# Kernel optimization log

Measured on AMD Instinct MI355X. Metric: run time of the kernel, lower is better.

Reference implementation:

```python
import jax, jax.numpy as jnp
import numpy as np

B, I, P, H = 256, 1024, 128, 128
L_PROT = 1024
ATOMS_PER_MOL = 128
N_LIG = B * ATOMS_PER_MOL  # 32768 total ligand atoms


def setup_inputs() -> dict:
    key = jax.random.key(0)
    ks = jax.random.split(key, 6)
    param_enc = jax.random.normal(ks[0], (B, I, P), dtype=jnp.float32)
    h_prot = jax.random.normal(ks[1], (B, L_PROT, H), dtype=jnp.float32)
    w1 = jax.random.normal(ks[2], (P, 1), dtype=jnp.float32) / np.sqrt(P)
    b1 = jax.random.normal(ks[3], (1,), dtype=jnp.float32)
    indices_lig = jax.random.randint(ks[4], (B, I), 0, ATOMS_PER_MOL)
    indices_prot = jax.random.randint(ks[5], (B, I), 0, L_PROT)
    protein_idx = jnp.arange(B)            # complex b -> protein row b
    lig_offsets = jnp.arange(B) * ATOMS_PER_MOL  # 'split' cumulative atom offsets
    mask = jnp.ones((B, I), dtype=bool)    # valid (non -510 padded) interactions
    return {
        "param_enc": param_enc, "h_prot": h_prot, "w1": w1, "b1": b1,
        "indices_lig": indices_lig, "indices_prot": indices_prot,
        "protein_idx": protein_idx, "lig_offsets": lig_offsets, "mask": mask,
    }


def reference(param_enc, h_prot, w1, b1, indices_lig, indices_prot,
              protein_idx, lig_offsets, mask):
    # scalar gate per interaction: ReLU(Linear(param_enc))  (dropout = identity, eval mode)
    gate = jax.nn.relu(jnp.einsum("bip,po->bio", param_enc, w1) + b1)  # [B, I, 1]
    # gather protein residue features: h_prot[protein_idx[b], indices_prot[b,i], :]
    gathered = h_prot[protein_idx[:, None], indices_prot]              # [B, I, H]
    contrib = gate * gathered * mask[..., None]                        # [B, I, H]
    # scatter-add into per-ligand-atom accumulator at split + i_l
    glob = (lig_offsets[:, None] + indices_lig).reshape(-1)            # [B*I]
    protein_inter = jnp.zeros((N_LIG, H), dtype=contrib.dtype)
    protein_inter = protein_inter.at[glob].add(contrib.reshape(-1, H))
    return protein_inter
```

## Files before the change

### kernel.cpp

```cpp
#include <hip/hip_runtime.h>

#define B_ 256
#define I_ 1024
#define P_ 128
#define H_ 128
#define LP_ 1024

__global__ __launch_bounds__(1024) void fused_ile(
    const float* __restrict__ param_enc,
    const float* __restrict__ h_prot,
    const float* __restrict__ w1,
    const float* __restrict__ b1,
    const int* __restrict__ indices_lig,
    const int* __restrict__ indices_prot,
    const int* __restrict__ protein_idx,
    const int* __restrict__ lig_offsets,
    float* __restrict__ out)
{
    __shared__ float          s_gate[I_];
    __shared__ unsigned short s_ip[I_];
    __shared__ unsigned short s_items[I_];
    __shared__ int            s_cnt[128];
    __shared__ int            s_start[129];
    __shared__ int            s_cur[128];

    const int tid  = threadIdx.x;
    const int b    = blockIdx.x;
    const int lane = tid & 63;
    const int wave = tid >> 6;
    const int half = lane >> 5;
    const int sub  = lane & 31;
    const int halfIdx = wave * 2 + half;

    if (tid < 128) s_cnt[tid] = 0;

    const float bias = b1[0];
    const int pb = protein_idx[b];
    const float4 wv = *(const float4*)(w1 + sub * 4);

    const float* pe_b = param_enc + (size_t)b * I_ * P_;
    const float* hp_b = h_prot + (size_t)pb * LP_ * H_;
    const int* il_b = indices_lig + b * I_;
    const int* ip_b = indices_prot + b * I_;

    #pragma unroll 8
    for (int q = 0; q < 32; ++q) {
        const int p  = wave + q * 16;
        const int i0 = p * 2;
        float4 pv = *(const float4*)(pe_b + (size_t)i0 * P_ + lane * 4);
        float part = pv.x * wv.x + pv.y * wv.y + pv.z * wv.z + pv.w * wv.w;
        part += __shfl_xor(part, 1);
        part += __shfl_xor(part, 2);
        part += __shfl_xor(part, 4);
        part += __shfl_xor(part, 8);
        part += __shfl_xor(part, 16);
        if (sub == 0) s_gate[i0 + half] = part + bias;
    }
    __syncthreads();

    const int  my_il = il_b[tid];
    const int  my_ip = ip_b[tid];
    const bool live  = s_gate[tid] > 0.f;
    s_ip[tid] = (unsigned short)my_ip;
    if (live) atomicAdd(&s_cnt[my_il], 1);
    __syncthreads();

    if (wave == 0) {
        const int c0 = s_cnt[2 * lane];
        const int c1 = s_cnt[2 * lane + 1];
        int s = c0 + c1;
        #pragma unroll
        for (int d = 1; d < 64; d <<= 1) {
            int t = __shfl_up(s, d);
            if (lane >= d) s += t;
        }
        s_start[2 * lane]     = s - c0 - c1;
        s_start[2 * lane + 1] = s - c1;
        if (lane == 63) s_start[128] = s;
    }
    __syncthreads();
    if (tid < 128) s_cur[tid] = s_start[tid];
    __syncthreads();

    if (live) {
        const int pos = atomicAdd(&s_cur[my_il], 1);
        s_items[pos] = (unsigned short)tid;
    }
    __syncthreads();

    const int base = lig_offsets[b];
    int st[4], cn[4];
    #pragma unroll
    for (int rr = 0; rr < 4; ++rr) {
        const int a = halfIdx + rr * 32;
        st[rr] = s_start[a];
        cn[rr] = s_start[a + 1] - st[rr];
    }
    float4 acc[4];
    #pragma unroll
    for (int rr = 0; rr < 4; ++rr) acc[rr] = make_float4(0.f, 0.f, 0.f, 0.f);

    int mx = max(max(cn[0], cn[1]), max(cn[2], cn[3]));
    for (int j = 0; j < mx; ++j) {
        #pragma unroll
        for (int rr = 0; rr < 4; ++rr) {
            if (j < cn[rr]) {
                const int   item = s_items[st[rr] + j];
                const float g    = s_gate[item];
                const int   ip   = s_ip[item];
                const float4 hv  = *(const float4*)(hp_b + (size_t)ip * H_ + sub * 4);
                acc[rr].x += g * hv.x;
                acc[rr].y += g * hv.y;
                acc[rr].z += g * hv.z;
                acc[rr].w += g * hv.w;
            }
        }
    }

    #pragma unroll
    for (int rr = 0; rr < 4; ++rr) {
        float* o = out + (size_t)(base + halfIdx + rr * 32) * H_;
        *(float4*)(o + sub * 4) = acc[rr];
    }
}

extern "C" void kernel_launch(void* const* d_in, const int* in_sizes, int n_in,
                              void* d_out, int out_size, void* d_ws, size_t ws_size,
                              hipStream_t stream) {
    const float* param_enc   = (const float*)d_in[0];
    const float* h_prot      = (const float*)d_in[1];
    const float* w1          = (const float*)d_in[2];
    const float* b1          = (const float*)d_in[3];
    const int* indices_lig   = (const int*)d_in[4];
    const int* indices_prot  = (const int*)d_in[5];
    const int* protein_idx   = (const int*)d_in[6];
    const int* lig_offsets   = (const int*)d_in[7];
    float* out = (float*)d_out;

    fused_ile<<<B_, 1024, 0, stream>>>(param_enc, h_prot, w1, b1,
                                       indices_lig, indices_prot,
                                       protein_idx, lig_offsets, out);
}
```

Measured before the change: 276.6 us.

## Split fused kernel into gate GEMV and per-segment sort-gather kernels

Replaces the single kernel (256 blocks of 1024 threads) with two launches. A GEMV kernel with 2048 blocks of 256 threads writes the gates to workspace. A sort-gather kernel with 1024 blocks of 256 threads then has each block handle one 32-atom segment of a molecule. The aim is more blocks for occupancy and load balance across CUs on a 256-block grid. The costs are a round trip of the gates through global memory, a second launch, and each segment block rereading all 1024 interaction indices and gates.

```diff
diff --git a/kernel.cpp b/kernel.cpp
--- a/kernel.cpp
+++ b/kernel.cpp
@@ -5,6 +5,151 @@
 #define P_ 128
 #define H_ 128
 #define LP_ 1024
+
+__global__ __launch_bounds__(256) void gates_gemv(
+    const float* __restrict__ param_enc,
+    const float* __restrict__ w1,
+    const float* __restrict__ b1,
+    float* __restrict__ gates)
+{
+    const int tid  = threadIdx.x;
+    const int lane = tid & 63;
+    const int wave = tid >> 6;
+    const int half = lane >> 5;
+    const int sub  = lane & 31;
+    const int w    = blockIdx.x * 4 + wave;
+    const int b    = w >> 5;
+    const int wwb  = w & 31;
+
+    const float bias = b1[0];
+    const float4 wv = *(const float4*)(w1 + sub * 4);
+    const float* pe_b = param_enc + (size_t)b * I_ * P_;
+    float* g_b = gates + b * I_;
+
+    #pragma unroll 8
+    for (int q = 0; q < 16; ++q) {
+        const int i0 = (wwb + q * 32) * 2;
+        float4 pv = *(const float4*)(pe_b + (size_t)i0 * P_ + lane * 4);
+        float part = pv.x * wv.x + pv.y * wv.y + pv.z * wv.z + pv.w * wv.w;
+        part += __shfl_xor(part, 1);
+        part += __shfl_xor(part, 2);
+        part += __shfl_xor(part, 4);
+        part += __shfl_xor(part, 8);
+        part += __shfl_xor(part, 16);
+        if (sub == 0) g_b[i0 + half] = part + bias;
+    }
+}
+
+__global__ __launch_bounds__(256) void sort_gather(
+    const float* __restrict__ gates,
+    const float* __restrict__ h_prot,
+    const int* __restrict__ indices_lig,
+    const int* __restrict__ indices_prot,
+    const int* __restrict__ protein_idx,
+    const int* __restrict__ lig_offsets,
+    float* __restrict__ out)
+{
+    __shared__ float          s_g[I_];
+    __shared__ unsigned short s_ipl[I_];
+    __shared__ unsigned short s_items[I_];
+    __shared__ int            s_cnt[32];
+    __shared__ int            s_start[33];
+    __shared__ int            s_cur[32];
+
+    const int tid  = threadIdx.x;
+    const int blk  = blockIdx.x;
+    const int b    = blk >> 2;
+    const int rseg = (blk & 3) << 5;
+    const int lane = tid & 63;
+    const int wave = tid >> 6;
+    const int half = lane >> 5;
+    const int sub  = lane & 31;
+    const int halfIdx = wave * 2 + half;
+
+    if (tid < 32) s_cnt[tid] = 0;
+
+    const int pb = protein_idx[b];
+    const float* hp_b = h_prot + (size_t)pb * LP_ * H_;
+    const float* g_b  = gates + b * I_;
+    const int* il_b   = indices_lig + b * I_;
+    const int* ip_b   = indices_prot + b * I_;
+
+    __syncthreads();
+
+    int  rloc[4];
+    bool lv[4];
+    #pragma unroll
+    for (int k = 0; k < 4; ++k) {
+        const int i  = tid + k * 256;
+        const float g = g_b[i];
+        const int il  = il_b[i];
+        const int ip  = ip_b[i];
+        s_g[i]   = g;
+        s_ipl[i] = (unsigned short)ip;
+        const int r = il - rseg;
+        lv[k]   = (g > 0.f) && ((unsigned)r < 32u);
+        rloc[k] = r;
+        if (lv[k]) atomicAdd(&s_cnt[r], 1);
+    }
+    __syncthreads();
+
+    if (wave == 0) {
+        const int c = (lane < 32) ? s_cnt[lane] : 0;
+        int s = c;
+        #pragma unroll
+        for (int d = 1; d < 32; d <<= 1) {
+            const int t = __shfl_up(s, d);
+            if (lane >= d) s += t;
+        }
+        if (lane < 32) { s_start[lane] = s - c; s_cur[lane] = s - c; }
+        if (lane == 31) s_start[32] = s;
+    }
+    __syncthreads();
+
+    #pragma unroll
+    for (int k = 0; k < 4; ++k) {
+        if (lv[k]) {
+            const int pos = atomicAdd(&s_cur[rloc[k]], 1);
+            s_items[pos] = (unsigned short)(tid + k * 256);
+        }
+    }
+    __syncthreads();
+
+    int st[4], cn[4];
+    #pragma unroll
+    for (int rr = 0; rr < 4; ++rr) {
+        const int a = halfIdx + rr * 8;
+        st[rr] = s_start[a];
+        cn[rr] = s_start[a + 1] - st[rr];
+    }
+    float4 acc[4];
+    #pragma unroll
+    for (int rr = 0; rr < 4; ++rr) acc[rr] = make_float4(0.f, 0.f, 0.f, 0.f);
+
+    const int mx = max(max(cn[0], cn[1]), max(cn[2], cn[3]));
+    for (int j = 0; j < mx; ++j) {
+        #pragma unroll
+        for (int rr = 0; rr < 4; ++rr) {
+            if (j < cn[rr]) {
+                const int   item = s_items[st[rr] + j];
+                const float g    = s_g[item];
+                const int   ip   = s_ipl[item];
+                const float4 hv  = *(const float4*)(hp_b + (size_t)ip * H_ + sub * 4);
+                acc[rr].x += g * hv.x;
+                acc[rr].y += g * hv.y;
+                acc[rr].z += g * hv.z;
+                acc[rr].w += g * hv.w;
+            }
+        }
+    }
+
+    const int base = lig_offsets[b] + rseg;
+    #pragma unroll
+    for (int rr = 0; rr < 4; ++rr) {
+        float* o = out + (size_t)(base + halfIdx + rr * 8) * H_;
+        *(float4*)(o + sub * 4) = acc[rr];
+    }
+}
 
 __global__ __launch_bounds__(1024) void fused_ile(
     const float* __restrict__ param_enc,
@@ -137,7 +282,16 @@
     const int* lig_offsets   = (const int*)d_in[7];
     float* out = (float*)d_out;
 
-    fused_ile<<<B_, 1024, 0, stream>>>(param_enc, h_prot, w1, b1,
-                                       indices_lig, indices_prot,
-                                       protein_idx, lig_offsets, out);
-}
+    const size_t gates_bytes = (size_t)B_ * I_ * sizeof(float);
+    if (ws_size >= gates_bytes && d_ws != nullptr) {
+        float* gates = (float*)d_ws;
+        gates_gemv<<<B_ * 8, 256, 0, stream>>>(param_enc, w1, b1, gates);
+        sort_gather<<<B_ * 4, 256, 0, stream>>>(gates, h_prot,
+                                                indices_lig, indices_prot,
+                                                protein_idx, lig_offsets, out);
+    } else {
+        fused_ile<<<B_, 1024, 0, stream>>>(param_enc, h_prot, w1, b1,
+                                           indices_lig, indices_prot,
+                                           protein_idx, lig_offsets, out);
+    }
+}
```

Result: slower. 283.9 us (+2.7%).
